# Optimization experiments

Hardware: AMD Instinct MI355X
Metric: run time of the kernel (lower is better)

The kernel has to match this reference:

```python
import jax, jax.numpy as jnp
import numpy as np


def setup_inputs() -> dict:
    key = jax.random.key(0)
    k1, k2 = jax.random.split(key)
    B, C, H, W_, P = 32, 256, 64, 64, 8
    x = jax.random.normal(k1, (B, C, H, W_), dtype=jnp.float32)
    # 1x1 conv weight [P, C] and bias [P], init like torch Conv2d default
    bound = 1.0 / np.sqrt(C)
    W = jax.random.uniform(k2, (P, C), dtype=jnp.float32, minval=-bound, maxval=bound)
    b = jnp.zeros((P,), dtype=jnp.float32)
    return {"x": x, "W": W, "b": b}


def reference(x, W, b):
    B, C, H, Wd = x.shape
    P = W.shape[0]
    # 1x1 conv: scores[b,p,h,w] = sum_c W[p,c] * x[b,c,h,w] + b[p]
    scores = jnp.einsum('pc,bchw->bphw', W, x) + b[None, :, None, None]
    # spatial softmax over HW
    part_maps = jax.nn.softmax(scores.reshape(B, P, H * Wd), axis=2).reshape(B, P, H, Wd)
    # fused per-part weighted average pool: mean over HW of x * map
    pooled = jnp.einsum('bchw,bphw->bpc', x, part_maps) / (H * Wd)  # [B,P,C]
    return pooled.reshape(B, P * C)
```

## Files before the change

kernel.cpp:

```cpp
#include <hip/hip_runtime.h>

#define HW 4096
#define NC 256
#define NP 8
#define NB 32
#define CHW 64
#define NCH 64

#define FMA4(acc, v, s)                  \
  acc.x = fmaf((v).x, (s), acc.x);       \
  acc.y = fmaf((v).y, (s), acc.y);       \
  acc.z = fmaf((v).z, (s), acc.z);       \
  acc.w = fmaf((v).w, (s), acc.w)

#define WT(c, pp) wt_els[(c) * NP + (pp)]
#define ELS(pp, hw) wt_els[(pp) * 64 + (hw)]

#define A_BATCH(xvarr, hbase)                                  \
  _Pragma("unroll")                                            \
  for (int i = 0; i < 8; ++i) {                                \
    int c = c0 + (hbase) + i * 4 + cr;                         \
    float4 wA = *(const float4*)&WT(c, 0);                     \
    float4 wB = *(const float4*)&WT(c, 4);                     \
    FMA4(s4[0], xvarr[i], wA.x);                               \
    FMA4(s4[1], xvarr[i], wA.y);                               \
    FMA4(s4[2], xvarr[i], wA.z);                               \
    FMA4(s4[3], xvarr[i], wA.w);                               \
    FMA4(s4[4], xvarr[i], wB.x);                               \
    FMA4(s4[5], xvarr[i], wB.y);                               \
    FMA4(s4[6], xvarr[i], wB.z);                               \
    FMA4(s4[7], xvarr[i], wB.w);                               \
  }

__global__ __launch_bounds__(256) void k_fused(
    const float* __restrict__ x, const float* __restrict__ Wm,
    const float* __restrict__ bias, float* __restrict__ partial,
    float* __restrict__ psum) {
  __shared__ __align__(16) float xs[NC][64];
  __shared__ __align__(16) float sp[4][NP][CHW];
  __shared__ __align__(16) float wt_els[NC * NP];

  const int bid = blockIdx.x;
  const int b = bid >> 6;
  const int chunk = bid & 63;
  const int t = threadIdx.x, lane = t & 63, w = t >> 6;
  const float* xb = x + (size_t)b * NC * HW + chunk * CHW;

#pragma unroll
  for (int p = 0; p < NP; ++p) WT(t, p) = Wm[p * NC + t];
  __syncthreads();

  const int cr = lane >> 4;
  const int q = lane & 15;
  const int c0 = w << 6;
  const float* xwp = xb + (size_t)(c0 + cr) * HW + q * 4;

  float4 s4[NP];
#pragma unroll
  for (int p = 0; p < NP; ++p) s4[p] = make_float4(0.f, 0.f, 0.f, 0.f);

#pragma unroll
  for (int h = 0; h < 2; ++h) {
    float4 xv[8];
#pragma unroll
    for (int i = 0; i < 8; ++i)
      xv[i] = *(const float4*)(xwp + (size_t)(h * 32 + i * 4) * HW);
#pragma unroll
    for (int i = 0; i < 8; ++i) {
      int c = c0 + h * 32 + i * 4 + cr;
      *(float4*)&xs[c][(q ^ (c & 7)) << 2] = xv[i];
    }
    A_BATCH(xv, h * 32)
  }

#pragma unroll
  for (int p = 0; p < NP; ++p) {
    float4 v = s4[p];
    v.x += __shfl_xor(v.x, 16); v.y += __shfl_xor(v.y, 16);
    v.z += __shfl_xor(v.z, 16); v.w += __shfl_xor(v.w, 16);
    v.x += __shfl_xor(v.x, 32); v.y += __shfl_xor(v.y, 32);
    v.z += __shfl_xor(v.z, 32); v.w += __shfl_xor(v.w, 32);
    if (cr == 0) *(float4*)&sp[w][p][q * 4] = v;
  }
  __syncthreads();

  {
    const int ep = t >> 5, eh = t & 31;
    float a0 = bias[ep], a1 = a0;
#pragma unroll
    for (int ww = 0; ww < 4; ++ww) {
      a0 += sp[ww][ep][eh];
      a1 += sp[ww][ep][eh + 32];
    }
    float e0 = expf(a0), e1 = expf(a1);
    ELS(ep, eh) = e0;
    ELS(ep, eh + 32) = e1;
    float esum = e0 + e1;
#pragma unroll
    for (int off = 16; off; off >>= 1) esum += __shfl_xor(esum, off);
    if (eh == 0) psum[bid * NP + ep] = esum;
  }
  __syncthreads();

  const int tk = t & 7;
  float acc[NP];
#pragma unroll
  for (int p = 0; p < NP; ++p) acc[p] = 0.f;

#pragma unroll
  for (int h = 0; h < 2; ++h) {
    float4 xv[8];
#pragma unroll
    for (int j = 0; j < 8; ++j) {
      int k = h * 8 + j;
      xv[j] = *(const float4*)&xs[t][(k ^ tk) << 2];
    }
#pragma unroll
    for (int j = 0; j < 8; ++j) {
      const int k = h * 8 + j;
#pragma unroll
      for (int p = 0; p < NP; ++p) {
        float4 e4 = *(const float4*)&ELS(p, k * 4);
        acc[p] = fmaf(xv[j].x, e4.x, acc[p]);
        acc[p] = fmaf(xv[j].y, e4.y, acc[p]);
        acc[p] = fmaf(xv[j].z, e4.z, acc[p]);
        acc[p] = fmaf(xv[j].w, e4.w, acc[p]);
      }
    }
  }

#pragma unroll
  for (int p = 0; p < NP; ++p)
    partial[((size_t)bid * NP + p) * NC + t] = acc[p];
}

__global__ __launch_bounds__(256) void k_reduce(
    const float* __restrict__ partial, const float* __restrict__ psum,
    float* __restrict__ out) {
  int bp = blockIdx.x;
  int b = bp >> 3, p = bp & 7;
  int t = threadIdx.x, lane = t & 63, w2 = t >> 6;

  __shared__ float gv;
  if (w2 == 0) {
    float v = psum[(size_t)(b * NCH + lane) * NP + p];
#pragma unroll
    for (int off = 32; off; off >>= 1) v += __shfl_xor(v, off);
    if (lane == 0) gv = 1.0f / (v * (float)HW);
  }
  __syncthreads();
  float ginv = gv;

  float acc = 0.f;
#pragma unroll 16
  for (int ch = 0; ch < NCH; ++ch)
    acc += partial[(((size_t)b * NCH + ch) * NP + p) * NC + t];
  out[((size_t)b * NP + p) * NC + t] = acc * ginv;
}

extern "C" void kernel_launch(void* const* d_in, const int* in_sizes, int n_in,
                              void* d_out, int out_size, void* d_ws, size_t ws_size,
                              hipStream_t stream) {
  const float* x = (const float*)d_in[0];
  const float* Wm = (const float*)d_in[1];
  const float* bias = (const float*)d_in[2];
  float* out = (float*)d_out;

  float* ws = (float*)d_ws;
  float* partial = ws;
  float* psum = ws + (size_t)NB * NCH * NP * NC;

  k_fused<<<NB * NCH, 256, 0, stream>>>(x, Wm, bias, partial, psum);
  k_reduce<<<NB * NP, 256, 0, stream>>>(partial, psum, out);
}
```

Baseline: 48.22 us.

## Replace partial-sum buffer with atomic accumulation and issue all x loads upfront

Each block now atomically adds its per-chunk pooled sums into a small per-batch accumulator instead of writing a full partial buffer that a second kernel must reduce. The reduce kernel becomes a light normalization pass, and a memset is added to zero the accumulator. The first stage also issues all 16 x loads before computing, which raises in-flight memory traffic and register pressure. Atomics cause contention, since 64 blocks add to each output, and make float summation order nondeterministic.

```diff
diff --git a/kernel.cpp b/kernel.cpp
--- a/kernel.cpp
+++ b/kernel.cpp
@@ -16,25 +16,9 @@
 #define WT(c, pp) wt_els[(c) * NP + (pp)]
 #define ELS(pp, hw) wt_els[(pp) * 64 + (hw)]
 
-#define A_BATCH(xvarr, hbase)                                  \
-  _Pragma("unroll")                                            \
-  for (int i = 0; i < 8; ++i) {                                \
-    int c = c0 + (hbase) + i * 4 + cr;                         \
-    float4 wA = *(const float4*)&WT(c, 0);                     \
-    float4 wB = *(const float4*)&WT(c, 4);                     \
-    FMA4(s4[0], xvarr[i], wA.x);                               \
-    FMA4(s4[1], xvarr[i], wA.y);                               \
-    FMA4(s4[2], xvarr[i], wA.z);                               \
-    FMA4(s4[3], xvarr[i], wA.w);                               \
-    FMA4(s4[4], xvarr[i], wB.x);                               \
-    FMA4(s4[5], xvarr[i], wB.y);                               \
-    FMA4(s4[6], xvarr[i], wB.z);                               \
-    FMA4(s4[7], xvarr[i], wB.w);                               \
-  }
-
 __global__ __launch_bounds__(256) void k_fused(
     const float* __restrict__ x, const float* __restrict__ Wm,
-    const float* __restrict__ bias, float* __restrict__ partial,
+    const float* __restrict__ bias, float* __restrict__ accw,
     float* __restrict__ psum) {
   __shared__ __align__(16) float xs[NC][64];
   __shared__ __align__(16) float sp[4][NP][CHW];
@@ -59,18 +43,27 @@
 #pragma unroll
   for (int p = 0; p < NP; ++p) s4[p] = make_float4(0.f, 0.f, 0.f, 0.f);
 
+  {
+    float4 xv[16];
 #pragma unroll
-  for (int h = 0; h < 2; ++h) {
-    float4 xv[8];
+    for (int i = 0; i < 16; ++i)
+      xv[i] = *(const float4*)(xwp + (size_t)(i * 4) * HW);
+
 #pragma unroll
-    for (int i = 0; i < 8; ++i)
-      xv[i] = *(const float4*)(xwp + (size_t)(h * 32 + i * 4) * HW);
-#pragma unroll
-    for (int i = 0; i < 8; ++i) {
-      int c = c0 + h * 32 + i * 4 + cr;
+    for (int i = 0; i < 16; ++i) {
+      int c = c0 + i * 4 + cr;
       *(float4*)&xs[c][(q ^ (c & 7)) << 2] = xv[i];
+      float4 wA = *(const float4*)&WT(c, 0);
+      float4 wB = *(const float4*)&WT(c, 4);
+      FMA4(s4[0], xv[i], wA.x);
+      FMA4(s4[1], xv[i], wA.y);
+      FMA4(s4[2], xv[i], wA.z);
+      FMA4(s4[3], xv[i], wA.w);
+      FMA4(s4[4], xv[i], wB.x);
+      FMA4(s4[5], xv[i], wB.y);
+      FMA4(s4[6], xv[i], wB.z);
+      FMA4(s4[7], xv[i], wB.w);
     }
-    A_BATCH(xv, h * 32)
   }
 
 #pragma unroll
@@ -131,31 +124,33 @@
 
 #pragma unroll
   for (int p = 0; p < NP; ++p)
-    partial[((size_t)bid * NP + p) * NC + t] = acc[p];
+    atomicAdd(&accw[(size_t)b * NP * NC + p * NC + t], acc[p]);
 }
 
-__global__ __launch_bounds__(256) void k_reduce(
-    const float* __restrict__ partial, const float* __restrict__ psum,
+__global__ __launch_bounds__(256) void k_norm(
+    const float* __restrict__ accw, const float* __restrict__ psum,
     float* __restrict__ out) {
-  int bp = blockIdx.x;
-  int b = bp >> 3, p = bp & 7;
-  int t = threadIdx.x, lane = t & 63, w2 = t >> 6;
+  __shared__ float gv[NP];
+  const int b = blockIdx.x;
+  const int t = threadIdx.x, lane = t & 63, w2 = t >> 6;
 
-  __shared__ float gv;
   if (w2 == 0) {
-    float v = psum[(size_t)(b * NCH + lane) * NP + p];
 #pragma unroll
-    for (int off = 32; off; off >>= 1) v += __shfl_xor(v, off);
-    if (lane == 0) gv = 1.0f / (v * (float)HW);
+    for (int p = 0; p < NP; ++p) {
+      float v = psum[(size_t)(b * NCH + lane) * NP + p];
+#pragma unroll
+      for (int off = 32; off; off >>= 1) v += __shfl_xor(v, off);
+      if (lane == 0) gv[p] = 1.0f / (v * (float)HW);
+    }
   }
   __syncthreads();
-  float ginv = gv;
 
-  float acc = 0.f;
-#pragma unroll 16
-  for (int ch = 0; ch < NCH; ++ch)
-    acc += partial[(((size_t)b * NCH + ch) * NP + p) * NC + t];
-  out[((size_t)b * NP + p) * NC + t] = acc * ginv;
+#pragma unroll
+  for (int it = 0; it < NP; ++it) {
+    int e = it * 256 + t;
+    int p = e >> 8;
+    out[(size_t)b * NP * NC + e] = accw[(size_t)b * NP * NC + e] * gv[p];
+  }
 }
 
 extern "C" void kernel_launch(void* const* d_in, const int* in_sizes, int n_in,
@@ -167,9 +162,10 @@
   float* out = (float*)d_out;
 
   float* ws = (float*)d_ws;
-  float* partial = ws;
-  float* psum = ws + (size_t)NB * NCH * NP * NC;
+  float* accw = ws;
+  float* psum = ws + (size_t)NB * NP * NC;
 
-  k_fused<<<NB * NCH, 256, 0, stream>>>(x, Wm, bias, partial, psum);
-  k_reduce<<<NB * NP, 256, 0, stream>>>(partial, psum, out);
+  hipMemsetAsync(accw, 0, (size_t)NB * NP * NC * sizeof(float), stream);
+  k_fused<<<NB * NCH, 256, 0, stream>>>(x, Wm, bias, accw, psum);
+  k_norm<<<NB, 256, 0, stream>>>(accw, psum, out);
 }
```

After: 53.30 us. 1.11x slower.
